# Kernel optimization log

Hardware: AMD Instinct MI355X
Metric: run time of the kernel (lower is better)

Reference implementation:

```python
import jax, jax.numpy as jnp
import numpy as np

B, N, C = 16, 196608, 2

def setup_inputs() -> dict:
    key = jax.random.key(0)
    k1, k2, k3, k4, k5 = jax.random.split(key, 5)
    return {
        "r": jax.random.normal(k1, (B, N, C), dtype=jnp.float32),
        "w": jax.random.uniform(k2, (B, N, 2), dtype=jnp.float32),
        "J_p": jax.random.normal(k3, (B, N, C, 6), dtype=jnp.float32),
        "J_d": jax.random.uniform(k4, (B, N, C, 1), dtype=jnp.float32),
        "lmbda": jax.random.uniform(k5, (B, 1, 1), dtype=jnp.float32),
    }

def reference(r, w, J_p, J_d, lmbda):
    # r: (B,N,C)  w: (B,N,2)  J_p: (B,N,C,6)  J_d: (B,N,C,1)  lmbda: (B,1,1)
    conf = w[..., 0:1]                                  # (B,N,1)
    node_lambda = w[..., 1:2]                           # (B,N,1)
    conf4 = conf[..., None]                             # (B,N,1,1)
    Jd = J_d[..., 0]                                    # (B,N,C)

    # Gauss-Newton blocks (sum-over-N reductions of tiny outer products)
    H_pp = jnp.einsum('bnki,bnkj->bij', J_p, conf4 * J_p)        # (B,6,6)
    H_pd = jnp.einsum('bnki,bnkj->bnij', J_p, conf4 * J_d)       # (B,N,6,1)
    H_dd = jnp.einsum('bnk,bnk->bn', Jd, conf * Jd)[..., None]   # (B,N,1)
    wr = conf * r                                                # (B,N,C)
    g_p = jnp.einsum('bnki,bnk->bi', J_p, wr)[..., None]         # (B,6,1)
    g_d = jnp.einsum('bnk,bnk->bn', Jd, wr)[..., None]           # (B,N,1)

    eye6 = jnp.eye(6, dtype=H_pp.dtype)[None]                    # (1,6,6)
    H_pp = H_pp + lmbda * eye6                                   # LM damping on pose block

    # Depth block damping + safe inverse
    H_dd_safe = jnp.maximum(H_dd + lmbda + node_lambda, 1e-4)    # (B,N,1)
    inv_H_dd = 1.0 / H_dd_safe                                   # (B,N,1)

    # Schur complement: H_eff = H_pp - sum_n H_pd invHdd H_pd^T
    H_pd_invHdd = H_pd * inv_H_dd[..., None]                     # (B,N,6,1)
    term = jnp.einsum('bnik,bnjk->bij', H_pd_invHdd, H_pd)       # (B,6,6)
    H_eff = H_pp - term + (0.01 + 0.001) * eye6                  # eye*0.01 then ridge 0.001
    g_eff = g_p - jnp.sum(H_pd_invHdd * g_d[..., None], axis=1)  # (B,6,1)

    delta_pose = jnp.linalg.solve(H_eff, g_eff)                  # (B,6,1)
    dp = delta_pose[..., 0]                                      # (B,6)

    # Back-substitute depths
    v = jnp.einsum('bnij,bi->bnj', H_pd, dp)                     # (B,N,1)
    delta_depth = inv_H_dd * (g_d - v)                           # (B,N,1)

    delta_pose_out = jnp.clip(dp, -2.0, 2.0)                     # (B,6)
    return (delta_pose_out, delta_depth)
```

## Files before the change

### kernel.cpp

```cpp
#include <hip/hip_runtime.h>


using f4 = __attribute__((ext_vector_type(4))) float;
using f2 = __attribute__((ext_vector_type(2))) float;

__device__ __forceinline__ f4 ntload4(const f4* p) {
    return __builtin_nontemporal_load(p);
}

constexpr int NACC = 27;

__device__ __forceinline__ void accum_point(
    const float ja[6], const float jb[6],
    float r0, float r1, float conf, float nlam, float jd0, float jd1,
    float lam, float* __restrict__ A, float* __restrict__ g)
{
    float h[6], gp[6];
#pragma unroll
    for (int i = 0; i < 6; ++i) {
        h[i]  = conf * (ja[i] * jd0 + jb[i] * jd1);
        gp[i] = conf * (ja[i] * r0 + jb[i] * r1);
    }
    const float hdd = conf * (jd0 * jd0 + jd1 * jd1);
    const float inv = 1.0f / fmaxf(hdd + lam + nlam, 1e-4f);
    const float gd  = conf * (jd0 * r0 + jd1 * r1);
    const float gdinv = gd * inv;
    int idx = 0;
#pragma unroll
    for (int i = 0; i < 6; ++i) {
        const float hii = h[i] * inv;
#pragma unroll
        for (int j = i; j < 6; ++j) {
            A[idx] += conf * (ja[i] * ja[j] + jb[i] * jb[j]) - hii * h[j];
            ++idx;
        }
        g[i] += gp[i] - h[i] * gdinv;
    }
}

constexpr int LDS_PITCH = 65;
constexpr int LDS_WAVE  = 6 * LDS_PITCH;

__device__ __forceinline__ void lds_fence()
{
    asm volatile("s_waitcnt lgkmcnt(0)" ::: "memory");
    __builtin_amdgcn_sched_barrier(0);
}

__global__ __launch_bounds__(256) void dba_reduce(
    const float* __restrict__ r, const float* __restrict__ w,
    const float* __restrict__ J_p, const float* __restrict__ J_d,
    const float* __restrict__ lmbda, float* __restrict__ acc, int N)
{
    __shared__ f4 sJ[4][LDS_WAVE];
    const int b = blockIdx.y;
    const float lam = lmbda[b];
    const int lane = threadIdx.x & 63;
    const int wave = threadIdx.x >> 6;
    f4* __restrict__ ldsW = sJ[wave];

    float A[21];
    float g[6];
#pragma unroll
    for (int i = 0; i < 21; ++i) A[i] = 0.f;
#pragma unroll
    for (int i = 0; i < 6; ++i) g[i] = 0.f;

    const size_t basePt = (size_t)b * (size_t)N;
    const int P  = N >> 1;
    const int PF = P & ~63;

    const f4* __restrict__ r4  = (const f4*)r   + (basePt >> 1);
    const f4* __restrict__ w4  = (const f4*)w   + (basePt >> 1);
    const f4* __restrict__ jd4 = (const f4*)J_d + (basePt >> 1);
    const f4* __restrict__ jp4 = (const f4*)J_p + basePt * 3;

    const int gw = blockIdx.x * 4 + wave;
    const int step = (gridDim.x * 4) << 6;

    f4* wadr[6];
#pragma unroll
    for (int k = 0; k < 6; ++k) {
        const int gg = (k << 6) + lane;
        const int p = gg / 6;
        const int s = gg - p * 6;
        wadr[k] = &ldsW[s * LDS_PITCH + p];
    }
    const f4* radr0 = &ldsW[0 * LDS_PITCH + lane];
    const f4* radr1 = &ldsW[1 * LDS_PITCH + lane];
    const f4* radr2 = &ldsW[2 * LDS_PITCH + lane];
    const f4* radr3 = &ldsW[3 * LDS_PITCH + lane];
    const f4* radr4 = &ldsW[4 * LDS_PITCH + lane];
    const f4* radr5 = &ldsW[5 * LDS_PITCH + lane];

    int pr0 = gw << 6;
    if (pr0 < PF) {
        const f4* jps = jp4 + (size_t)pr0 * 6;
        f4 c_rv = ntload4(r4 + pr0 + lane);
        f4 c_wv = ntload4(w4 + pr0 + lane);
        f4 c_jd = ntload4(jd4 + pr0 + lane);
        f4 c_q0 = ntload4(jps + 0 * 64 + lane);
        f4 c_q1 = ntload4(jps + 1 * 64 + lane);
        f4 c_q2 = ntload4(jps + 2 * 64 + lane);
        f4 c_q3 = ntload4(jps + 3 * 64 + lane);
        f4 c_q4 = ntload4(jps + 4 * 64 + lane);
        f4 c_q5 = ntload4(jps + 5 * 64 + lane);

        for (; pr0 < PF; pr0 += step) {
            const int nxt = (pr0 + step < PF) ? (pr0 + step) : pr0;
            const f4* jpn = jp4 + (size_t)nxt * 6;
            f4 n_rv = ntload4(r4 + nxt + lane);
            f4 n_wv = ntload4(w4 + nxt + lane);
            f4 n_jd = ntload4(jd4 + nxt + lane);
            f4 n_q0 = ntload4(jpn + 0 * 64 + lane);
            f4 n_q1 = ntload4(jpn + 1 * 64 + lane);
            f4 n_q2 = ntload4(jpn + 2 * 64 + lane);
            f4 n_q3 = ntload4(jpn + 3 * 64 + lane);
            f4 n_q4 = ntload4(jpn + 4 * 64 + lane);
            f4 n_q5 = ntload4(jpn + 5 * 64 + lane);

            *wadr[0] = c_q0;
            *wadr[1] = c_q1;
            *wadr[2] = c_q2;
            *wadr[3] = c_q3;
            *wadr[4] = c_q4;
            *wadr[5] = c_q5;
            lds_fence();

            {
                const f4 J0 = *radr0;
                const f4 J1 = *radr1;
                const f4 J2 = *radr2;
                const float ja[6] = {J0[0], J0[1], J0[2], J0[3], J1[0], J1[1]};
                const float jb[6] = {J1[2], J1[3], J2[0], J2[1], J2[2], J2[3]};
                accum_point(ja, jb, c_rv[0], c_rv[1], c_wv[0], c_wv[1],
                            c_jd[0], c_jd[1], lam, A, g);
            }
            {
                const f4 J3 = *radr3;
                const f4 J4 = *radr4;
                const f4 J5 = *radr5;
                const float ja[6] = {J3[0], J3[1], J3[2], J3[3], J4[0], J4[1]};
                const float jb[6] = {J4[2], J4[3], J5[0], J5[1], J5[2], J5[3]};
                accum_point(ja, jb, c_rv[2], c_rv[3], c_wv[2], c_wv[3],
                            c_jd[2], c_jd[3], lam, A, g);
            }

            c_rv = n_rv; c_wv = n_wv; c_jd = n_jd;
            c_q0 = n_q0; c_q1 = n_q1; c_q2 = n_q2;
            c_q3 = n_q3; c_q4 = n_q4; c_q5 = n_q5;
        }
    }

    for (int pr = PF + (int)(blockIdx.x * blockDim.x + threadIdx.x); pr < P;
         pr += (int)(gridDim.x * blockDim.x)) {
        const size_t pt = basePt + ((size_t)pr << 1);
        const float4 rv = *(const float4*)(r + pt * 2);
        const float4 wv = *(const float4*)(w + pt * 2);
        const float4 jd = *(const float4*)(J_d + pt * 2);
        const float4* jp = (const float4*)(J_p + pt * 12);
        const float4 q0 = jp[0], q1 = jp[1], q2 = jp[2];
        const float4 q3 = jp[3], q4 = jp[4], q5 = jp[5];
        {
            const float ja[6] = {q0.x, q0.y, q0.z, q0.w, q1.x, q1.y};
            const float jb[6] = {q1.z, q1.w, q2.x, q2.y, q2.z, q2.w};
            accum_point(ja, jb, rv.x, rv.y, wv.x, wv.y, jd.x, jd.y, lam, A, g);
        }
        {
            const float ja[6] = {q3.x, q3.y, q3.z, q3.w, q4.x, q4.y};
            const float jb[6] = {q4.z, q4.w, q5.x, q5.y, q5.z, q5.w};
            accum_point(ja, jb, rv.z, rv.w, wv.z, wv.w, jd.z, jd.w, lam, A, g);
        }
    }

    float v[NACC];
#pragma unroll
    for (int i = 0; i < 21; ++i) v[i] = A[i];
#pragma unroll
    for (int i = 0; i < 6; ++i) v[21 + i] = g[i];

#pragma unroll
    for (int off = 32; off > 0; off >>= 1) {
#pragma unroll
        for (int i = 0; i < NACC; ++i) v[i] += __shfl_down(v[i], off, 64);
    }

    __shared__ float sred[4][NACC];
    if (lane == 0) {
#pragma unroll
        for (int i = 0; i < NACC; ++i) sred[wave][i] = v[i];
    }
    __syncthreads();
    if (threadIdx.x < NACC) {
        const float s = sred[0][threadIdx.x] + sred[1][threadIdx.x] +
                        sred[2][threadIdx.x] + sred[3][threadIdx.x];
        atomicAdd(&acc[b * 32 + threadIdx.x], s);
    }
}

__global__ void dba_solve(const float* __restrict__ acc,
                          const float* __restrict__ lmbda,
                          float* __restrict__ pose_out,
                          float* __restrict__ dp_ws, int B)
{
    const int b = blockIdx.x * blockDim.x + threadIdx.x;
    if (b >= B) return;
    float M[6][7];
    const float* a = acc + b * 32;
    int idx = 0;
#pragma unroll
    for (int i = 0; i < 6; ++i) {
#pragma unroll
        for (int j = i; j < 6; ++j) {
            const float t = a[idx++];
            M[i][j] = t;
            M[j][i] = t;
        }
    }
#pragma unroll
    for (int i = 0; i < 6; ++i) M[i][6] = a[21 + i];
    const float lam = lmbda[b];
#pragma unroll
    for (int i = 0; i < 6; ++i) M[i][i] += lam + 0.011f;

#pragma unroll
    for (int k = 0; k < 6; ++k) {
        const float piv = 1.0f / M[k][k];
#pragma unroll
        for (int j = 0; j < 7; ++j) M[k][j] *= piv;
#pragma unroll
        for (int i = 0; i < 6; ++i) {
            if (i == k) continue;
            const float f = M[i][k];
#pragma unroll
            for (int j = 0; j < 7; ++j) M[i][j] -= f * M[k][j];
        }
    }
#pragma unroll
    for (int i = 0; i < 6; ++i) {
        const float x = M[i][6];
        dp_ws[b * 6 + i] = x;
        pose_out[b * 6 + i] = fminf(fmaxf(x, -2.0f), 2.0f);
    }
}

__device__ __forceinline__ float depth_point(
    const float ja[6], const float jb[6], const float* __restrict__ dp,
    float r0, float r1, float conf, float nlam, float jd0, float jd1, float lam)
{
    float v = 0.f;
#pragma unroll
    for (int i = 0; i < 6; ++i)
        v += (ja[i] * jd0 + jb[i] * jd1) * dp[i];
    v *= conf;
    const float hdd = conf * (jd0 * jd0 + jd1 * jd1);
    const float inv = 1.0f / fmaxf(hdd + lam + nlam, 1e-4f);
    const float gd  = conf * (jd0 * r0 + jd1 * r1);
    return inv * (gd - v);
}

__global__ __launch_bounds__(256) void dba_depth(
    const float* __restrict__ r, const float* __restrict__ w,
    const float* __restrict__ J_p, const float* __restrict__ J_d,
    const float* __restrict__ lmbda, const float* __restrict__ dp_ws,
    float* __restrict__ depth_out, int N)
{
    __shared__ f4 sJ[4][LDS_WAVE];
    const int b = blockIdx.y;
    const float lam = lmbda[b];
    const int lane = threadIdx.x & 63;
    const int wave = threadIdx.x >> 6;
    f4* __restrict__ ldsW = sJ[wave];

    float dp[6];
#pragma unroll
    for (int i = 0; i < 6; ++i) dp[i] = dp_ws[b * 6 + i];

    const size_t basePt = (size_t)b * (size_t)N;
    const int P  = N >> 1;
    const int PF = P & ~63;

    const f4* __restrict__ r4  = (const f4*)r   + (basePt >> 1);
    const f4* __restrict__ w4  = (const f4*)w   + (basePt >> 1);
    const f4* __restrict__ jd4 = (const f4*)J_d + (basePt >> 1);
    const f4* __restrict__ jp4 = (const f4*)J_p + basePt * 3;
    f2* __restrict__ out2 = (f2*)depth_out + (basePt >> 1);

    const int gw = blockIdx.x * 4 + wave;
    const int step = (gridDim.x * 4) << 6;

    f4* wadr[6];
#pragma unroll
    for (int k = 0; k < 6; ++k) {
        const int gg = (k << 6) + lane;
        const int p = gg / 6;
        const int s = gg - p * 6;
        wadr[k] = &ldsW[s * LDS_PITCH + p];
    }
    const f4* radr0 = &ldsW[0 * LDS_PITCH + lane];
    const f4* radr1 = &ldsW[1 * LDS_PITCH + lane];
    const f4* radr2 = &ldsW[2 * LDS_PITCH + lane];
    const f4* radr3 = &ldsW[3 * LDS_PITCH + lane];
    const f4* radr4 = &ldsW[4 * LDS_PITCH + lane];
    const f4* radr5 = &ldsW[5 * LDS_PITCH + lane];

    int pr0 = gw << 6;
    if (pr0 < PF) {
        const f4* jps = jp4 + (size_t)pr0 * 6;
        f4 c_rv = ntload4(r4 + pr0 + lane);
        f4 c_wv = ntload4(w4 + pr0 + lane);
        f4 c_jd = ntload4(jd4 + pr0 + lane);
        f4 c_q0 = ntload4(jps + 0 * 64 + lane);
        f4 c_q1 = ntload4(jps + 1 * 64 + lane);
        f4 c_q2 = ntload4(jps + 2 * 64 + lane);
        f4 c_q3 = ntload4(jps + 3 * 64 + lane);
        f4 c_q4 = ntload4(jps + 4 * 64 + lane);
        f4 c_q5 = ntload4(jps + 5 * 64 + lane);

        for (; pr0 < PF; pr0 += step) {
            const int nxt = (pr0 + step < PF) ? (pr0 + step) : pr0;
            const f4* jpn = jp4 + (size_t)nxt * 6;
            f4 n_rv = ntload4(r4 + nxt + lane);
            f4 n_wv = ntload4(w4 + nxt + lane);
            f4 n_jd = ntload4(jd4 + nxt + lane);
            f4 n_q0 = ntload4(jpn + 0 * 64 + lane);
            f4 n_q1 = ntload4(jpn + 1 * 64 + lane);
            f4 n_q2 = ntload4(jpn + 2 * 64 + lane);
            f4 n_q3 = ntload4(jpn + 3 * 64 + lane);
            f4 n_q4 = ntload4(jpn + 4 * 64 + lane);
            f4 n_q5 = ntload4(jpn + 5 * 64 + lane);

            *wadr[0] = c_q0;
            *wadr[1] = c_q1;
            *wadr[2] = c_q2;
            *wadr[3] = c_q3;
            *wadr[4] = c_q4;
            *wadr[5] = c_q5;
            lds_fence();

            f2 outv;
            {
                const f4 J0 = *radr0;
                const f4 J1 = *radr1;
                const f4 J2 = *radr2;
                const float ja[6] = {J0[0], J0[1], J0[2], J0[3], J1[0], J1[1]};
                const float jb[6] = {J1[2], J1[3], J2[0], J2[1], J2[2], J2[3]};
                outv[0] = depth_point(ja, jb, dp, c_rv[0], c_rv[1], c_wv[0],
                                      c_wv[1], c_jd[0], c_jd[1], lam);
            }
            {
                const f4 J3 = *radr3;
                const f4 J4 = *radr4;
                const f4 J5 = *radr5;
                const float ja[6] = {J3[0], J3[1], J3[2], J3[3], J4[0], J4[1]};
                const float jb[6] = {J4[2], J4[3], J5[0], J5[1], J5[2], J5[3]};
                outv[1] = depth_point(ja, jb, dp, c_rv[2], c_rv[3], c_wv[2],
                                      c_wv[3], c_jd[2], c_jd[3], lam);
            }
            __builtin_nontemporal_store(outv, out2 + pr0 + lane);

            c_rv = n_rv; c_wv = n_wv; c_jd = n_jd;
            c_q0 = n_q0; c_q1 = n_q1; c_q2 = n_q2;
            c_q3 = n_q3; c_q4 = n_q4; c_q5 = n_q5;
        }
    }

    for (int pr = PF + (int)(blockIdx.x * blockDim.x + threadIdx.x); pr < P;
         pr += (int)(gridDim.x * blockDim.x)) {
        const size_t pt = basePt + ((size_t)pr << 1);
        const float4 rv = *(const float4*)(r + pt * 2);
        const float4 wv = *(const float4*)(w + pt * 2);
        const float4 jd = *(const float4*)(J_d + pt * 2);
        const float4* jp = (const float4*)(J_p + pt * 12);
        const float4 q0 = jp[0], q1 = jp[1], q2 = jp[2];
        const float4 q3 = jp[3], q4 = jp[4], q5 = jp[5];
        float2 outv;
        {
            const float ja[6] = {q0.x, q0.y, q0.z, q0.w, q1.x, q1.y};
            const float jb[6] = {q1.z, q1.w, q2.x, q2.y, q2.z, q2.w};
            outv.x = depth_point(ja, jb, dp, rv.x, rv.y, wv.x, wv.y, jd.x, jd.y, lam);
        }
        {
            const float ja[6] = {q3.x, q3.y, q3.z, q3.w, q4.x, q4.y};
            const float jb[6] = {q4.z, q4.w, q5.x, q5.y, q5.z, q5.w};
            outv.y = depth_point(ja, jb, dp, rv.z, rv.w, wv.z, wv.w, jd.z, jd.w, lam);
        }
        *(float2*)(depth_out + pt) = outv;
    }
}

extern "C" void kernel_launch(void* const* d_in, const int* in_sizes, int n_in,
                              void* d_out, int out_size, void* d_ws, size_t ws_size,
                              hipStream_t stream)
{
    const float* r   = (const float*)d_in[0];
    const float* w   = (const float*)d_in[1];
    const float* J_p = (const float*)d_in[2];
    const float* J_d = (const float*)d_in[3];
    const float* lmb = (const float*)d_in[4];
    const int B = in_sizes[4];
    const int N = in_sizes[0] / (B * 2);

    float* acc   = (float*)d_ws;
    float* dp_ws = (float*)d_ws + B * 32;
    float* out   = (float*)d_out;

    hipMemsetAsync(acc, 0, B * 32 * sizeof(float), stream);

    dim3 grid(96, B);
    dba_reduce<<<grid, 256, 0, stream>>>(r, w, J_p, J_d, lmb, acc, N);
    dba_solve<<<1, 64, 0, stream>>>(acc, lmb, out, dp_ws, B);
    dba_depth<<<grid, 256, 0, stream>>>(r, w, J_p, J_d, lmb, dp_ws, out + B * 6, N);
}
```

Measured before the change: 305.0 us.

## Cache per-point Schur terms in reduce pass for a lightweight depth back-substitution

The reduce kernel now writes seven per-point values (H_pd*invHdd for the six pose terms, plus g_d*invHdd) to a workspace cache, padded to 32 bytes per point. When the workspace is large enough, a new depth kernel reads only that cache instead of re-reading r, w, J_d and J_p, and computes each depth with a 6-term dot product. The aim is to cut the second full pass over the 72-byte-per-point inputs and the recomputation in the depth kernel. In exchange the reduce pass takes on extra write traffic, so the net memory saving is small. The fallback depth kernel is simplified to plain strided loads without the LDS transpose.

```diff
diff --git a/kernel.cpp b/kernel.cpp
--- a/kernel.cpp
+++ b/kernel.cpp
@@ -13,7 +13,8 @@
 __device__ __forceinline__ void accum_point(
     const float ja[6], const float jb[6],
     float r0, float r1, float conf, float nlam, float jd0, float jd1,
-    float lam, float* __restrict__ A, float* __restrict__ g)
+    float lam, float* __restrict__ A, float* __restrict__ g,
+    float* __restrict__ c7)
 {
     float h[6], gp[6];
 #pragma unroll
@@ -25,10 +26,12 @@
     const float inv = 1.0f / fmaxf(hdd + lam + nlam, 1e-4f);
     const float gd  = conf * (jd0 * r0 + jd1 * r1);
     const float gdinv = gd * inv;
+    c7[6] = gdinv;
     int idx = 0;
 #pragma unroll
     for (int i = 0; i < 6; ++i) {
         const float hii = h[i] * inv;
+        c7[i] = hii;
 #pragma unroll
         for (int j = i; j < 6; ++j) {
             A[idx] += conf * (ja[i] * ja[j] + jb[i] * jb[j]) - hii * h[j];
@@ -47,10 +50,19 @@
     __builtin_amdgcn_sched_barrier(0);
 }
 
+__device__ __forceinline__ void store_rec(f4* __restrict__ rec, const float* c7)
+{
+    f4 lo = {c7[0], c7[1], c7[2], c7[3]};
+    f4 hi = {c7[4], c7[5], c7[6], 0.f};
+    rec[0] = lo;
+    rec[1] = hi;
+}
+
 __global__ __launch_bounds__(256) void dba_reduce(
     const float* __restrict__ r, const float* __restrict__ w,
     const float* __restrict__ J_p, const float* __restrict__ J_d,
-    const float* __restrict__ lmbda, float* __restrict__ acc, int N)
+    const float* __restrict__ lmbda, float* __restrict__ acc,
+    float* __restrict__ cache, int do_cache, int N)
 {
     __shared__ f4 sJ[4][LDS_WAVE];
     const int b = blockIdx.y;
@@ -74,6 +86,7 @@
     const f4* __restrict__ w4  = (const f4*)w   + (basePt >> 1);
     const f4* __restrict__ jd4 = (const f4*)J_d + (basePt >> 1);
     const f4* __restrict__ jp4 = (const f4*)J_p + basePt * 3;
+    f4* __restrict__ cb = (f4*)cache + basePt * 2;
 
     const int gw = blockIdx.x * 4 + wave;
     const int step = (gridDim.x * 4) << 6;
@@ -127,6 +140,7 @@
             *wadr[5] = c_q5;
             lds_fence();
 
+            float c7a[7], c7b[7];
             {
                 const f4 J0 = *radr0;
                 const f4 J1 = *radr1;
@@ -134,7 +148,7 @@
                 const float ja[6] = {J0[0], J0[1], J0[2], J0[3], J1[0], J1[1]};
                 const float jb[6] = {J1[2], J1[3], J2[0], J2[1], J2[2], J2[3]};
                 accum_point(ja, jb, c_rv[0], c_rv[1], c_wv[0], c_wv[1],
-                            c_jd[0], c_jd[1], lam, A, g);
+                            c_jd[0], c_jd[1], lam, A, g, c7a);
             }
             {
                 const f4 J3 = *radr3;
@@ -143,7 +157,12 @@
                 const float ja[6] = {J3[0], J3[1], J3[2], J3[3], J4[0], J4[1]};
                 const float jb[6] = {J4[2], J4[3], J5[0], J5[1], J5[2], J5[3]};
                 accum_point(ja, jb, c_rv[2], c_rv[3], c_wv[2], c_wv[3],
-                            c_jd[2], c_jd[3], lam, A, g);
+                            c_jd[2], c_jd[3], lam, A, g, c7b);
+            }
+            if (do_cache) {
+                f4* rec = cb + (size_t)(pr0 + lane) * 4;
+                store_rec(rec + 0, c7a);
+                store_rec(rec + 2, c7b);
             }
 
             c_rv = n_rv; c_wv = n_wv; c_jd = n_jd;
@@ -161,15 +180,21 @@
         const float4* jp = (const float4*)(J_p + pt * 12);
         const float4 q0 = jp[0], q1 = jp[1], q2 = jp[2];
         const float4 q3 = jp[3], q4 = jp[4], q5 = jp[5];
+        float c7a[7], c7b[7];
         {
             const float ja[6] = {q0.x, q0.y, q0.z, q0.w, q1.x, q1.y};
             const float jb[6] = {q1.z, q1.w, q2.x, q2.y, q2.z, q2.w};
-            accum_point(ja, jb, rv.x, rv.y, wv.x, wv.y, jd.x, jd.y, lam, A, g);
+            accum_point(ja, jb, rv.x, rv.y, wv.x, wv.y, jd.x, jd.y, lam, A, g, c7a);
         }
         {
             const float ja[6] = {q3.x, q3.y, q3.z, q3.w, q4.x, q4.y};
             const float jb[6] = {q4.z, q4.w, q5.x, q5.y, q5.z, q5.w};
-            accum_point(ja, jb, rv.z, rv.w, wv.z, wv.w, jd.z, jd.w, lam, A, g);
+            accum_point(ja, jb, rv.z, rv.w, wv.z, wv.w, jd.z, jd.w, lam, A, g, c7b);
+        }
+        if (do_cache) {
+            f4* rec = cb + (size_t)pr * 4;
+            store_rec(rec + 0, c7a);
+            store_rec(rec + 2, c7b);
         }
     }
 
@@ -241,6 +266,35 @@
         const float x = M[i][6];
         dp_ws[b * 6 + i] = x;
         pose_out[b * 6 + i] = fminf(fmaxf(x, -2.0f), 2.0f);
+    }
+}
+
+__global__ __launch_bounds__(256) void dba_depth_cached(
+    const float* __restrict__ cache, const float* __restrict__ dp_ws,
+    float* __restrict__ depth_out, int N)
+{
+    const int b = blockIdx.y;
+    float dp[6];
+#pragma unroll
+    for (int i = 0; i < 6; ++i) dp[i] = dp_ws[b * 6 + i];
+
+    const size_t basePt = (size_t)b * (size_t)N;
+    const int P = N >> 1;
+    const f4* __restrict__ cb = (const f4*)cache + basePt * 2;
+    f2* __restrict__ out2 = (f2*)depth_out + (basePt >> 1);
+
+    for (int pr = blockIdx.x * blockDim.x + threadIdx.x; pr < P;
+         pr += gridDim.x * blockDim.x) {
+        const f4 c0 = cb[(size_t)pr * 4 + 0];
+        const f4 c1 = cb[(size_t)pr * 4 + 1];
+        const f4 c2 = cb[(size_t)pr * 4 + 2];
+        const f4 c3 = cb[(size_t)pr * 4 + 3];
+        f2 o;
+        o[0] = c1[2] - (c0[0] * dp[0] + c0[1] * dp[1] + c0[2] * dp[2] +
+                        c0[3] * dp[3] + c1[0] * dp[4] + c1[1] * dp[5]);
+        o[1] = c3[2] - (c2[0] * dp[0] + c2[1] * dp[1] + c2[2] * dp[2] +
+                        c2[3] * dp[3] + c3[0] * dp[4] + c3[1] * dp[5]);
+        out2[pr] = o;
     }
 }
 
@@ -259,114 +313,22 @@
     return inv * (gd - v);
 }
 
-__global__ __launch_bounds__(256) void dba_depth(
+__global__ __launch_bounds__(256) void dba_depth_full(
     const float* __restrict__ r, const float* __restrict__ w,
     const float* __restrict__ J_p, const float* __restrict__ J_d,
     const float* __restrict__ lmbda, const float* __restrict__ dp_ws,
     float* __restrict__ depth_out, int N)
 {
-    __shared__ f4 sJ[4][LDS_WAVE];
     const int b = blockIdx.y;
     const float lam = lmbda[b];
-    const int lane = threadIdx.x & 63;
-    const int wave = threadIdx.x >> 6;
-    f4* __restrict__ ldsW = sJ[wave];
-
     float dp[6];
 #pragma unroll
     for (int i = 0; i < 6; ++i) dp[i] = dp_ws[b * 6 + i];
 
     const size_t basePt = (size_t)b * (size_t)N;
-    const int P  = N >> 1;
-    const int PF = P & ~63;
-
-    const f4* __restrict__ r4  = (const f4*)r   + (basePt >> 1);
-    const f4* __restrict__ w4  = (const f4*)w   + (basePt >> 1);
-    const f4* __restrict__ jd4 = (const f4*)J_d + (basePt >> 1);
-    const f4* __restrict__ jp4 = (const f4*)J_p + basePt * 3;
-    f2* __restrict__ out2 = (f2*)depth_out + (basePt >> 1);
-
-    const int gw = blockIdx.x * 4 + wave;
-    const int step = (gridDim.x * 4) << 6;
-
-    f4* wadr[6];
-#pragma unroll
-    for (int k = 0; k < 6; ++k) {
-        const int gg = (k << 6) + lane;
-        const int p = gg / 6;
-        const int s = gg - p * 6;
-        wadr[k] = &ldsW[s * LDS_PITCH + p];
-    }
-    const f4* radr0 = &ldsW[0 * LDS_PITCH + lane];
-    const f4* radr1 = &ldsW[1 * LDS_PITCH + lane];
-    const f4* radr2 = &ldsW[2 * LDS_PITCH + lane];
-    const f4* radr3 = &ldsW[3 * LDS_PITCH + lane];
-    const f4* radr4 = &ldsW[4 * LDS_PITCH + lane];
-    const f4* radr5 = &ldsW[5 * LDS_PITCH + lane];
-
-    int pr0 = gw << 6;
-    if (pr0 < PF) {
-        const f4* jps = jp4 + (size_t)pr0 * 6;
-        f4 c_rv = ntload4(r4 + pr0 + lane);
-        f4 c_wv = ntload4(w4 + pr0 + lane);
-        f4 c_jd = ntload4(jd4 + pr0 + lane);
-        f4 c_q0 = ntload4(jps + 0 * 64 + lane);
-        f4 c_q1 = ntload4(jps + 1 * 64 + lane);
-        f4 c_q2 = ntload4(jps + 2 * 64 + lane);
-        f4 c_q3 = ntload4(jps + 3 * 64 + lane);
-        f4 c_q4 = ntload4(jps + 4 * 64 + lane);
-        f4 c_q5 = ntload4(jps + 5 * 64 + lane);
-
-        for (; pr0 < PF; pr0 += step) {
-            const int nxt = (pr0 + step < PF) ? (pr0 + step) : pr0;
-            const f4* jpn = jp4 + (size_t)nxt * 6;
-            f4 n_rv = ntload4(r4 + nxt + lane);
-            f4 n_wv = ntload4(w4 + nxt + lane);
-            f4 n_jd = ntload4(jd4 + nxt + lane);
-            f4 n_q0 = ntload4(jpn + 0 * 64 + lane);
-            f4 n_q1 = ntload4(jpn + 1 * 64 + lane);
-            f4 n_q2 = ntload4(jpn + 2 * 64 + lane);
-            f4 n_q3 = ntload4(jpn + 3 * 64 + lane);
-            f4 n_q4 = ntload4(jpn + 4 * 64 + lane);
-            f4 n_q5 = ntload4(jpn + 5 * 64 + lane);
-
-            *wadr[0] = c_q0;
-            *wadr[1] = c_q1;
-            *wadr[2] = c_q2;
-            *wadr[3] = c_q3;
-            *wadr[4] = c_q4;
-            *wadr[5] = c_q5;
-            lds_fence();
-
-            f2 outv;
-            {
-                const f4 J0 = *radr0;
-                const f4 J1 = *radr1;
-                const f4 J2 = *radr2;
-                const float ja[6] = {J0[0], J0[1], J0[2], J0[3], J1[0], J1[1]};
-                const float jb[6] = {J1[2], J1[3], J2[0], J2[1], J2[2], J2[3]};
-                outv[0] = depth_point(ja, jb, dp, c_rv[0], c_rv[1], c_wv[0],
-                                      c_wv[1], c_jd[0], c_jd[1], lam);
-            }
-            {
-                const f4 J3 = *radr3;
-                const f4 J4 = *radr4;
-                const f4 J5 = *radr5;
-                const float ja[6] = {J3[0], J3[1], J3[2], J3[3], J4[0], J4[1]};
-                const float jb[6] = {J4[2], J4[3], J5[0], J5[1], J5[2], J5[3]};
-                outv[1] = depth_point(ja, jb, dp, c_rv[2], c_rv[3], c_wv[2],
-                                      c_wv[3], c_jd[2], c_jd[3], lam);
-            }
-            __builtin_nontemporal_store(outv, out2 + pr0 + lane);
-
-            c_rv = n_rv; c_wv = n_wv; c_jd = n_jd;
-            c_q0 = n_q0; c_q1 = n_q1; c_q2 = n_q2;
-            c_q3 = n_q3; c_q4 = n_q4; c_q5 = n_q5;
-        }
-    }
-
-    for (int pr = PF + (int)(blockIdx.x * blockDim.x + threadIdx.x); pr < P;
-         pr += (int)(gridDim.x * blockDim.x)) {
+    const int P = N >> 1;
+    for (int pr = blockIdx.x * blockDim.x + threadIdx.x; pr < P;
+         pr += gridDim.x * blockDim.x) {
         const size_t pt = basePt + ((size_t)pr << 1);
         const float4 rv = *(const float4*)(r + pt * 2);
         const float4 wv = *(const float4*)(w + pt * 2);
@@ -402,13 +364,26 @@
     const int N = in_sizes[0] / (B * 2);
 
     float* acc   = (float*)d_ws;
-    float* dp_ws = (float*)d_ws + B * 32;
+    float* dp_ws = (float*)d_ws + 512;
+    float* cache = (float*)d_ws + 1024;
     float* out   = (float*)d_out;
 
+    const size_t cacheBytes = (size_t)B * (size_t)N * 32;
+    const int use_cache = (ws_size >= 4096 + cacheBytes) ? 1 : 0;
+
     hipMemsetAsync(acc, 0, B * 32 * sizeof(float), stream);
 
     dim3 grid(96, B);
-    dba_reduce<<<grid, 256, 0, stream>>>(r, w, J_p, J_d, lmb, acc, N);
+    dba_reduce<<<grid, 256, 0, stream>>>(r, w, J_p, J_d, lmb, acc,
+                                         cache, use_cache, N);
     dba_solve<<<1, 64, 0, stream>>>(acc, lmb, out, dp_ws, B);
-    dba_depth<<<grid, 256, 0, stream>>>(r, w, J_p, J_d, lmb, dp_ws, out + B * 6, N);
-}
+    if (use_cache) {
+        dim3 dgrid(192, B);
+        dba_depth_cached<<<dgrid, 256, 0, stream>>>(cache, dp_ws,
+                                                    out + B * 6, N);
+    } else {
+        dim3 dgrid(192, B);
+        dba_depth_full<<<dgrid, 256, 0, stream>>>(r, w, J_p, J_d, lmb, dp_ws,
+                                                  out + B * 6, N);
+    }
+}
```

Result: no change. 299.3 us (-1.9%).
